# Performance work log

Measured on AMD Instinct MI355X. Metric: run time of the kernel, lower is better.

The kernel has to match this reference:

```python
import jax, jax.numpy as jnp
import numpy as np

B, T, C = 8, 512, 512
H, HKV, D = 8, 4, 64
S_MAX = 128
BASE_FREQ = 10000.0
INIT_SIGMA = 256.0
EPS = 1e-6


def _init_positional_kernel(n_heads, head_dim, s_max, base_freq):
    table_size = 2 * s_max + 1
    deltas = jnp.arange(table_size) - s_max
    d_half = head_dim // 2
    freqs = 1.0 / base_freq ** (jnp.arange(d_half, dtype=jnp.float32) / d_half)
    phases = deltas[:, None].astype(jnp.float32) * freqs[None, :]
    P_single = jnp.concatenate([jnp.cos(phases), jnp.sin(phases)], axis=-1)
    return jnp.tile(P_single[None, :, :], (n_heads, 1, 1))


def setup_inputs() -> dict:
    key = jax.random.key(0)
    ks = jax.random.split(key, 6)
    scale = 0.02
    x = jax.random.normal(ks[0], (B, T, C), dtype=jnp.float32)
    Wq = jax.random.normal(ks[1], (C, H * D), dtype=jnp.float32) * scale
    Wk = jax.random.normal(ks[2], (C, HKV * D), dtype=jnp.float32) * scale
    Wv = jax.random.normal(ks[3], (C, HKV * D), dtype=jnp.float32) * scale
    Wproj = jax.random.normal(ks[4], (C, C), dtype=jnp.float32) * scale
    P = _init_positional_kernel(H, D, S_MAX, BASE_FREQ)
    sigma = jnp.full((H,), INIT_SIGMA, dtype=jnp.float32)
    return {"x": x, "Wq": Wq, "Wk": Wk, "Wv": Wv, "Wproj": Wproj, "P": P, "sigma": sigma}


def _norm(t):
    # nGPT-style: unit norm * sqrt(dim)
    dim = t.shape[-1]
    return t * (jnp.sqrt(float(dim)) * jax.lax.rsqrt((t * t).sum(axis=-1, keepdims=True) + EPS))


def _warped_kernel(P, sigma, T_):
    # P: [H, 2*S_MAX+1, D], sigma: [H] -> P_interp: [H, T, T, D]
    positions = jnp.arange(T_)
    delta = positions[:, None] - positions[None, :]  # [T, T]
    s = jnp.abs(sigma) + 1e-6
    delta_warped = S_MAX * jnp.tanh(delta[None, :, :].astype(jnp.float32) / s[:, None, None])
    delta_table = delta_warped + S_MAX  # [H, T, T]
    idx_lo = jnp.floor(delta_table).astype(jnp.int32)
    idx_hi = idx_lo + 1
    frac = delta_table - idx_lo.astype(P.dtype)
    table_max = 2 * S_MAX
    idx_lo = jnp.clip(idx_lo, 0, table_max)
    idx_hi = jnp.clip(idx_hi, 0, table_max)
    head_idx = jnp.arange(H)[:, None, None]
    P_lo = P[head_idx, idx_lo, :]  # [H, T, T, D]
    P_hi = P[head_idx, idx_hi, :]
    return (1 - frac[..., None]) * P_lo + frac[..., None] * P_hi


def reference(x, Wq, Wk, Wv, Wproj, P, sigma):
    q = (x @ Wq).reshape(B, T, H, D)
    k = (x @ Wk).reshape(B, T, HKV, D)
    v = (x @ Wv).reshape(B, T, HKV, D)
    q, k = _norm(q), _norm(k)
    repeats = H // HKV
    k = jnp.repeat(k, repeats, axis=2)
    v = jnp.repeat(v, repeats, axis=2)
    q = q.transpose(0, 2, 1, 3)  # [B, H, T, D]
    k = k.transpose(0, 2, 1, 3)
    v = v.transpose(0, 2, 1, 3)

    sm_scale = 1.0 / jnp.sqrt(float(D))
    P_interp = _warped_kernel(P, sigma, T)  # [H, T, T, D]
    S = jnp.einsum('bhid,hijd,bhjd->bhij', q, P_interp, k) * sm_scale
    causal_mask = jnp.tril(jnp.ones((T, T), dtype=jnp.bool_))
    S = jnp.where(causal_mask[None, None, :, :], S, jnp.finfo(S.dtype).min)
    A = jax.nn.softmax(S, axis=-1)
    y = A @ v  # [B, H, T, D]
    y = y.transpose(0, 2, 1, 3).reshape(B, T, H * D)
    return y @ Wproj
```

## Files before the change

kernel.cpp:

```cpp
#include <hip/hip_runtime.h>
#include <hip/hip_bf16.h>
#include <math.h>

#define Bb 8
#define Tt 512
#define Cc 512
#define Hh 8
#define HKV 4
#define Dd 64

typedef __attribute__((ext_vector_type(8))) short short8;
typedef __attribute__((ext_vector_type(4))) float float4v;
typedef __attribute__((ext_vector_type(2))) __fp16 h2;
typedef __attribute__((ext_vector_type(8))) __fp16 half8;

__device__ __forceinline__ h2 u2h(unsigned u) {
  union { unsigned u; h2 h; } x; x.u = u; return x.h;
}
__device__ __forceinline__ unsigned h2u(h2 h) {
  union { h2 h; unsigned u; } x; x.h = h; return x.u;
}
__device__ __forceinline__ float fdot2(h2 a, h2 b, float c) {
#if __has_builtin(__builtin_amdgcn_fdot2)
  return __builtin_amdgcn_fdot2(a, b, c, false);
#else
  return fmaf((float)a.x, (float)b.x, fmaf((float)a.y, (float)b.y, c));
#endif
}

__device__ __forceinline__ float wave_reduce_sum(float v) {
#pragma unroll
  for (int off = 32; off > 0; off >>= 1) v += __shfl_xor(v, off, 64);
  return v;
}
__device__ __forceinline__ unsigned pack_bf2(float a, float b) {
  __hip_bfloat162 h = __float22bfloat162_rn(make_float2(a, b));
  return *(unsigned*)&h;
}

__global__ __launch_bounds__(256) void prep(
    const float* __restrict__ x, const float* __restrict__ Wq,
    const float* __restrict__ Wk, const float* __restrict__ Wv,
    const float* __restrict__ Wp, const float* __restrict__ P,
    const float* __restrict__ sigma,
    unsigned short* __restrict__ xb, unsigned short* __restrict__ Wtq,
    unsigned short* __restrict__ Wtp, unsigned short* __restrict__ Pwh) {
  const int bid = blockIdx.x;
  const int t = threadIdx.x;
  if (bid < 1024) {
    int i = (bid * 256 + t) * 8;
    float4 f0 = *(const float4*)&x[i];
    float4 f1 = *(const float4*)&x[i + 4];
    unsigned u[4] = {pack_bf2(f0.x, f0.y), pack_bf2(f0.z, f0.w),
                     pack_bf2(f1.x, f1.y), pack_bf2(f1.z, f1.w)};
    *(uint4*)&xb[i] = *(uint4*)u;
  } else if (bid < 1216) {
    __shared__ float Ts[64][65];
    const int bx = bid - 1024;
    const int k0 = (bx & 7) << 6;
    const int n0 = (bx >> 3) << 6;
    const float* src; int ld, nc0; unsigned short* dst; int ndst;
    if (n0 < 512)       { src = Wq; ld = 512; nc0 = n0;        dst = Wtq; ndst = n0; }
    else if (n0 < 768)  { src = Wk; ld = 256; nc0 = n0 - 512;  dst = Wtq; ndst = n0; }
    else if (n0 < 1024) { src = Wv; ld = 256; nc0 = n0 - 768;  dst = Wtq; ndst = n0; }
    else                { src = Wp; ld = 512; nc0 = n0 - 1024; dst = Wtp; ndst = n0 - 1024; }
    const int r = t >> 4, c4 = (t & 15) << 2;
#pragma unroll
    for (int rr = 0; rr < 4; ++rr) {
      int row = (rr << 4) + r;
      float4 f = *(const float4*)&src[(k0 + row) * ld + nc0 + c4];
      Ts[row][c4] = f.x; Ts[row][c4 + 1] = f.y;
      Ts[row][c4 + 2] = f.z; Ts[row][c4 + 3] = f.w;
    }
    __syncthreads();
#pragma unroll
    for (int rr = 0; rr < 4; ++rr) {
      int nr = (rr << 4) + r;
      unsigned u0 = pack_bf2(Ts[c4][nr], Ts[c4 + 1][nr]);
      unsigned u1 = pack_bf2(Ts[c4 + 2][nr], Ts[c4 + 3][nr]);
      *(uint2*)&dst[(ndst + nr) * 512 + k0 + c4] = make_uint2(u0, u1);
    }
  } else {
    int idx = (bid - 1216) * 256 + t;
    int d = idx & 63;
    int rem = idx >> 6;
    int dd = rem % 1023;
    int h = rem / 1023;
    float s = fabsf(sigma[h]) + 1e-6f;
    float delta = (float)(dd - 511);
    float dt = 128.0f * tanhf(delta / s) + 128.0f;
    float lo = floorf(dt);
    int ilo = (int)lo;
    float frac = dt - lo;
    ilo = max(0, min(ilo, 256));
    int ihi = min(ilo + 1, 256);
    const float* Pb = P + h * 257 * 64;
    float val = (1.0f - frac) * Pb[ilo * 64 + d] + frac * Pb[ihi * 64 + d];
    __fp16 hv = (__fp16)val;
    Pwh[idx] = *(unsigned short*)&hv;
  }
}

__global__ __launch_bounds__(256) void qkv_mfma(
    const unsigned short* __restrict__ xb, const unsigned short* __restrict__ Wt,
    unsigned short* __restrict__ qh, unsigned short* __restrict__ kh,
    unsigned short* __restrict__ vT) {
  __shared__ unsigned short As[64][72];
  __shared__ unsigned short Bs[64][72];
  const int m0 = blockIdx.x * 64;
  const int n0 = blockIdx.y * 64;
  const int t = threadIdx.x;
  const int w = t >> 6, lane = t & 63;
  const int srow = t >> 2, sc = (t & 3) << 4;
  float4v acc[4] = {{0,0,0,0},{0,0,0,0},{0,0,0,0},{0,0,0,0}};
  for (int k0 = 0; k0 < 512; k0 += 64) {
    uint4 a0 = *(const uint4*)&xb[(m0 + srow) * 512 + k0 + sc];
    uint4 a1 = *(const uint4*)&xb[(m0 + srow) * 512 + k0 + sc + 8];
    uint4 b0 = *(const uint4*)&Wt[(n0 + srow) * 512 + k0 + sc];
    uint4 b1 = *(const uint4*)&Wt[(n0 + srow) * 512 + k0 + sc + 8];
    __syncthreads();
    *(uint4*)&As[srow][sc] = a0; *(uint4*)&As[srow][sc + 8] = a1;
    *(uint4*)&Bs[srow][sc] = b0; *(uint4*)&Bs[srow][sc + 8] = b1;
    __syncthreads();
    const int ml = (w << 4) + (lane & 15);
    const int kq = (lane >> 4) << 3;
    short8 aF0 = *(short8*)&As[ml][kq];
    short8 aF1 = *(short8*)&As[ml][kq + 32];
#pragma unroll
    for (int nt = 0; nt < 4; ++nt) {
      const int nl = (nt << 4) + (lane & 15);
      short8 bF0 = *(short8*)&Bs[nl][kq];
      short8 bF1 = *(short8*)&Bs[nl][kq + 32];
      acc[nt] = __builtin_amdgcn_mfma_f32_16x16x32_bf16(aF0, bF0, acc[nt], 0, 0, 0);
      acc[nt] = __builtin_amdgcn_mfma_f32_16x16x32_bf16(aF1, bF1, acc[nt], 0, 0, 0);
    }
  }
  const int lane15 = lane & 15;
  const int rowbase = m0 + (w << 4) + ((lane >> 4) << 2);
  if (n0 < 768) {
#pragma unroll
    for (int r = 0; r < 4; ++r) {
      float ss = 0.0f;
#pragma unroll
      for (int nt = 0; nt < 4; ++nt) ss = fmaf(acc[nt][r], acc[nt][r], ss);
#pragma unroll
      for (int off = 1; off < 16; off <<= 1) ss += __shfl_xor(ss, off, 64);
      float sc2 = 8.0f * rsqrtf(ss + 1e-6f);
      const int row = rowbase + r;
      if (n0 < 512) {
        const int h = n0 >> 6;
        const float sc3 = sc2 * 0.125f;
#pragma unroll
        for (int nt = 0; nt < 4; ++nt) {
          __fp16 hv = (__fp16)(acc[nt][r] * sc3);
          qh[(row * Hh + h) * Dd + (nt << 4) + lane15] = *(unsigned short*)&hv;
        }
      } else {
        const int hkv = (n0 - 512) >> 6;
#pragma unroll
        for (int nt = 0; nt < 4; ++nt) {
          __fp16 hv = (__fp16)(acc[nt][r] * sc2);
          kh[(row * HKV + hkv) * Dd + (nt << 4) + lane15] = *(unsigned short*)&hv;
        }
      }
    }
  } else {
    const int hkv = (n0 - 768) >> 6;
    const int bb = rowbase >> 9;
    const int trow = rowbase & 511;
#pragma unroll
    for (int nt = 0; nt < 4; ++nt) {
      const int d = (nt << 4) + lane15;
      unsigned u0 = h2u(__builtin_amdgcn_cvt_pkrtz(acc[nt][0], acc[nt][1]));
      unsigned u1 = h2u(__builtin_amdgcn_cvt_pkrtz(acc[nt][2], acc[nt][3]));
      *(uint2*)&vT[((bb * HKV + hkv) * 64 + d) * 512 + trow] = make_uint2(u0, u1);
    }
  }
}

__global__ __launch_bounds__(256) void proj_mfma(
    const unsigned short* __restrict__ yb, const unsigned short* __restrict__ Wt,
    float* __restrict__ out) {
  __shared__ unsigned short As[64][72];
  __shared__ unsigned short Bs[64][72];
  const int m0 = blockIdx.x * 64;
  const int n0 = blockIdx.y * 64;
  const int t = threadIdx.x;
  const int w = t >> 6, lane = t & 63;
  const int srow = t >> 2, sc = (t & 3) << 4;
  float4v acc[4] = {{0,0,0,0},{0,0,0,0},{0,0,0,0},{0,0,0,0}};
  for (int k0 = 0; k0 < 512; k0 += 64) {
    uint4 a0 = *(const uint4*)&yb[(m0 + srow) * 512 + k0 + sc];
    uint4 a1 = *(const uint4*)&yb[(m0 + srow) * 512 + k0 + sc + 8];
    uint4 b0 = *(const uint4*)&Wt[(n0 + srow) * 512 + k0 + sc];
    uint4 b1 = *(const uint4*)&Wt[(n0 + srow) * 512 + k0 + sc + 8];
    __syncthreads();
    *(uint4*)&As[srow][sc] = a0; *(uint4*)&As[srow][sc + 8] = a1;
    *(uint4*)&Bs[srow][sc] = b0; *(uint4*)&Bs[srow][sc + 8] = b1;
    __syncthreads();
    const int ml = (w << 4) + (lane & 15);
    const int kq = (lane >> 4) << 3;
    short8 aF0 = *(short8*)&As[ml][kq];
    short8 aF1 = *(short8*)&As[ml][kq + 32];
#pragma unroll
    for (int nt = 0; nt < 4; ++nt) {
      const int nl = (nt << 4) + (lane & 15);
      short8 bF0 = *(short8*)&Bs[nl][kq];
      short8 bF1 = *(short8*)&Bs[nl][kq + 32];
      acc[nt] = __builtin_amdgcn_mfma_f32_16x16x32_bf16(aF0, bF0, acc[nt], 0, 0, 0);
      acc[nt] = __builtin_amdgcn_mfma_f32_16x16x32_bf16(aF1, bF1, acc[nt], 0, 0, 0);
    }
  }
#pragma unroll
  for (int nt = 0; nt < 4; ++nt) {
    int col = n0 + (nt << 4) + (lane & 15);
#pragma unroll
    for (int r = 0; r < 4; ++r) {
      int row = m0 + (w << 4) + ((lane >> 4) << 2) + r;
      out[row * 512 + col] = acc[nt][r];
    }
  }
}

__global__ __launch_bounds__(256) void attn(
    const unsigned short* __restrict__ qh, const unsigned short* __restrict__ kh,
    const unsigned short* __restrict__ vT, const unsigned short* __restrict__ Pwh,
    unsigned short* __restrict__ yb) {
  __shared__ __fp16 PwS[96][72];
  __shared__ __fp16 pS[32][72];
  __shared__ float lS[32];

  const int t = threadIdx.x;
  const int lane = t & 63;
  const int wu = __builtin_amdgcn_readfirstlane(t >> 6);
  const int bh = blockIdx.x;
  const int b = bh >> 3;
  const int h = bh & 7;
  const int hkv = h >> 1;
  const int i0 = (int)((0x4567BA983210CDEFull >> (blockIdx.y * 4)) & 15) * 32;

  float l_lane[8];
#pragma unroll
  for (int r = 0; r < 8; ++r) l_lane[r] = 0.0f;
  float4v oacc[2] = {{0, 0, 0, 0}, {0, 0, 0, 0}};

  const int prow = (wu << 3) + 63 - lane;
  const int i_base = i0 + (wu << 3);
  const unsigned short* qbase = &qh[((b * Tt + i_base) * Hh + h) * Dd];

  const int i16 = (wu & 1) << 4;
  const int dt0 = (wu >> 1) << 1;
  const int lm = lane & 15;
  const int kq = (lane >> 4) << 3;
  const unsigned short* vTbase = &vT[((b * HKV + hkv) * 64) * 512];

  for (int jt0 = 0; jt0 <= i0 + 31; jt0 += 64) {
    __syncthreads();
    {
      int jr = t >> 2, dc = (t & 3) << 4;
      const int pb0 = h * 1023 + (i0 - jt0) + 448;
      const unsigned short* pwp = &Pwh[(pb0 + jr) * 64 + dc];
      *(uint4*)&PwS[jr][dc]     = *(const uint4*)&pwp[0];
      *(uint4*)&PwS[jr][dc + 8] = *(const uint4*)&pwp[8];
      int pr2 = 64 + (t >> 3), dc2 = (t & 7) << 3;
      if (pr2 < 95)
        *(uint4*)&PwS[pr2][dc2] = *(const uint4*)&Pwh[(pb0 + pr2) * 64 + dc2];
    }
    uint4 kr[8];
    {
      const uint4* kp = (const uint4*)&kh[((b * Tt + jt0 + lane) * HKV + hkv) * Dd];
#pragma unroll
      for (int c = 0; c < 8; ++c) kr[c] = kp[c];
    }
    __syncthreads();

    const int j = jt0 + lane;
#pragma unroll
    for (int r = 0; r < 8; ++r) {
      const uint4* qp = (const uint4*)&qbase[r * (Hh * Dd)];
      float srx = 0.0f, sry = 0.0f, srz = 0.0f, srw = 0.0f;
#pragma unroll
      for (int ch = 0; ch < 8; ++ch) {
        uint4 qu = qp[ch];
        uint4 pu = *(uint4*)&PwS[prow + r][ch << 3];
        srx = fdot2(u2h(qu.x) * u2h(pu.x), u2h(kr[ch].x), srx);
        sry = fdot2(u2h(qu.y) * u2h(pu.y), u2h(kr[ch].y), sry);
        srz = fdot2(u2h(qu.z) * u2h(pu.z), u2h(kr[ch].z), srz);
        srw = fdot2(u2h(qu.w) * u2h(pu.w), u2h(kr[ch].w), srw);
      }
      float sr = (srx + sry) + (srz + srw);
      float sv = (j <= i_base + r) ? sr : -1e30f;
      float p = __expf(sv - 6.0f);
      l_lane[r] += p;
      pS[(wu << 3) + r][lane] = (__fp16)p;
    }
    __syncthreads();

    half8 a0 = *(half8*)&pS[i16 + lm][kq];
    half8 a1 = *(half8*)&pS[i16 + lm][kq + 32];
#pragma unroll
    for (int dd = 0; dd < 2; ++dd) {
      const unsigned short* vp = vTbase + (((dt0 + dd) << 4) + lm) * 512 + jt0 + kq;
      half8 b0 = *(const half8*)&vp[0];
      half8 b1 = *(const half8*)&vp[32];
      oacc[dd] = __builtin_amdgcn_mfma_f32_16x16x32_f16(a0, b0, oacc[dd], 0, 0, 0);
      oacc[dd] = __builtin_amdgcn_mfma_f32_16x16x32_f16(a1, b1, oacc[dd], 0, 0, 0);
    }
  }

#pragma unroll
  for (int r = 0; r < 8; ++r) {
    float lr = wave_reduce_sum(l_lane[r]);
    if (lane == r) lS[(wu << 3) + r] = lr;
  }
  __syncthreads();

#pragma unroll
  for (int dd = 0; dd < 2; ++dd) {
    const int d = ((dt0 + dd) << 4) + lm;
#pragma unroll
    for (int r = 0; r < 4; ++r) {
      const int irow = i16 + ((lane >> 4) << 2) + r;
      const float val = oacc[dd][r] / lS[irow];
      __hip_bfloat16 hv = __float2bfloat16(val);
      yb[((b * Tt + i0 + irow) * Hh + h) * Dd + d] = *(unsigned short*)&hv;
    }
  }
}

extern "C" void kernel_launch(void* const* d_in, const int* in_sizes, int n_in,
                              void* d_out, int out_size, void* d_ws, size_t ws_size,
                              hipStream_t stream) {
  const float* x     = (const float*)d_in[0];
  const float* Wq    = (const float*)d_in[1];
  const float* Wk    = (const float*)d_in[2];
  const float* Wv    = (const float*)d_in[3];
  const float* Wproj = (const float*)d_in[4];
  const float* P     = (const float*)d_in[5];
  const float* sigma = (const float*)d_in[6];
  float* out = (float*)d_out;

  float* ws = (float*)d_ws;
  unsigned short* qh  = (unsigned short*)ws;
  unsigned short* kh  = (unsigned short*)(ws + 1048576);
  unsigned short* vT  = (unsigned short*)(ws + 1572864);
  unsigned short* Pwh = (unsigned short*)(ws + 2097152);
  unsigned short* xb  = (unsigned short*)(ws + 2359296);
  unsigned short* yb  = xb;
  unsigned short* Wtq = (unsigned short*)(ws + 3407872);
  unsigned short* Wtp = (unsigned short*)(ws + 3670016);

  prep<<<dim3(3262), 256, 0, stream>>>(x, Wq, Wk, Wv, Wproj, P, sigma,
                                       xb, Wtq, Wtp, Pwh);
  qkv_mfma<<<dim3(64, 16), 256, 0, stream>>>(xb, Wtq, qh, kh, vT);
  attn<<<dim3(64, 16), 256, 0, stream>>>(qh, kh, vT, Pwh, yb);
  proj_mfma<<<dim3(64, 8), 256, 0, stream>>>(yb, Wtp, out);
}
```

Before: 137.6 us.

## Split long causal attention rows across two blocks and merge partial sums

Query tiles in the upper half of the sequence (yp ≥ 8) now have their key range split between two blocks. A constant table assigns each blockIdx.y a query tile, a starting key tile and a key-tile count, which caps per-block work at four key tiles instead of up to eight. Split blocks write unnormalized partial outputs and row sums to scratch space, reusing the output buffer and the no-longer-needed weight workspace. A new merge kernel adds the two halves and normalizes. The attention kernel also gets an occupancy hint of 8 blocks per SM. The aim is to remove the causal load imbalance at the tail, at the cost of an extra launch and extra global traffic for the partials.

```diff
diff --git a/kernel.cpp b/kernel.cpp
--- a/kernel.cpp
+++ b/kernel.cpp
@@ -37,6 +37,17 @@
   __hip_bfloat162 h = __float22bfloat162_rn(make_float2(a, b));
   return *(unsigned*)&h;
 }
+
+__constant__ unsigned ATAB[24] = {
+  0x04000F, 0x04000E, 0x04040F, 0x04040E, 0x04000D, 0x04000C,
+  0x03040D, 0x03040C, 0x03000B, 0x03000A, 0x03030B, 0x03030A,
+  0x030009, 0x030008,
+  0x040007, 0x040006,
+  0x020309, 0x020308,
+  0x030005, 0x030004,
+  0x020003, 0x020002,
+  0x010001, 0x010000
+};
 
 __global__ __launch_bounds__(256) void prep(
     const float* __restrict__ x, const float* __restrict__ Wq,
@@ -222,10 +233,11 @@
   }
 }
 
-__global__ __launch_bounds__(256) void attn(
+__global__ __launch_bounds__(256, 8) void attn(
     const unsigned short* __restrict__ qh, const unsigned short* __restrict__ kh,
     const unsigned short* __restrict__ vT, const unsigned short* __restrict__ Pwh,
-    unsigned short* __restrict__ yb) {
+    unsigned short* __restrict__ yb, float* __restrict__ opart,
+    float* __restrict__ lpart) {
   __shared__ __fp16 PwS[96][72];
   __shared__ __fp16 pS[32][72];
   __shared__ float lS[32];
@@ -237,7 +249,11 @@
   const int b = bh >> 3;
   const int h = bh & 7;
   const int hkv = h >> 1;
-  const int i0 = (int)((0x4567BA983210CDEFull >> (blockIdx.y * 4)) & 15) * 32;
+  const unsigned ae = ATAB[blockIdx.y];
+  const int yp  = ae & 255;
+  const int jts = (ae >> 8) & 255;
+  const int njt = (ae >> 16) & 255;
+  const int i0 = yp << 5;
 
   float l_lane[8];
 #pragma unroll
@@ -254,7 +270,8 @@
   const int kq = (lane >> 4) << 3;
   const unsigned short* vTbase = &vT[((b * HKV + hkv) * 64) * 512];
 
-  for (int jt0 = 0; jt0 <= i0 + 31; jt0 += 64) {
+  for (int jt = jts; jt < jts + njt; ++jt) {
+    const int jt0 = jt << 6;
     __syncthreads();
     {
       int jr = t >> 2, dc = (t & 3) << 4;
@@ -315,17 +332,58 @@
   }
   __syncthreads();
 
-#pragma unroll
-  for (int dd = 0; dd < 2; ++dd) {
-    const int d = ((dt0 + dd) << 4) + lm;
-#pragma unroll
-    for (int r = 0; r < 4; ++r) {
-      const int irow = i16 + ((lane >> 4) << 2) + r;
-      const float val = oacc[dd][r] / lS[irow];
-      __hip_bfloat16 hv = __float2bfloat16(val);
-      yb[((b * Tt + i0 + irow) * Hh + h) * Dd + d] = *(unsigned short*)&hv;
-    }
-  }
+  if (yp >= 8) {
+    const int slot = (jts != 0);
+    const int pbase = (((bh << 3) + (yp - 8)) << 1) + slot;
+    float* ob = opart + pbase * 2048;
+#pragma unroll
+    for (int dd = 0; dd < 2; ++dd) {
+      const int d = ((dt0 + dd) << 4) + lm;
+#pragma unroll
+      for (int r = 0; r < 4; ++r) {
+        const int irow = i16 + ((lane >> 4) << 2) + r;
+        ob[irow * 64 + d] = oacc[dd][r];
+      }
+    }
+    if (t < 32) lpart[pbase * 32 + t] = lS[t];
+  } else {
+#pragma unroll
+    for (int dd = 0; dd < 2; ++dd) {
+      const int d = ((dt0 + dd) << 4) + lm;
+#pragma unroll
+      for (int r = 0; r < 4; ++r) {
+        const int irow = i16 + ((lane >> 4) << 2) + r;
+        const float val = oacc[dd][r] / lS[irow];
+        __hip_bfloat16 hv = __float2bfloat16(val);
+        yb[((b * Tt + i0 + irow) * Hh + h) * Dd + d] = *(unsigned short*)&hv;
+      }
+    }
+  }
+}
+
+__global__ __launch_bounds__(256) void merge(
+    const float* __restrict__ opart, const float* __restrict__ lpart,
+    unsigned short* __restrict__ yb) {
+  const int bt = blockIdx.x;
+  const int bh = bt >> 3;
+  const int b = bh >> 3, h = bh & 7;
+  const int i0 = ((bt & 7) + 8) << 5;
+  const int t = threadIdx.x;
+  const int row = t >> 3;
+  const int d0 = (t & 7) << 3;
+  const float* oA = opart + (bt << 1) * 2048;
+  const float* oB = oA + 2048;
+  const float linv = 1.0f / (lpart[(bt << 1) * 32 + row] + lpart[((bt << 1) + 1) * 32 + row]);
+  float4 a0 = *(const float4*)&oA[row * 64 + d0];
+  float4 a1 = *(const float4*)&oA[row * 64 + d0 + 4];
+  float4 b0 = *(const float4*)&oB[row * 64 + d0];
+  float4 b1 = *(const float4*)&oB[row * 64 + d0 + 4];
+  unsigned u[4];
+  u[0] = pack_bf2((a0.x + b0.x) * linv, (a0.y + b0.y) * linv);
+  u[1] = pack_bf2((a0.z + b0.z) * linv, (a0.w + b0.w) * linv);
+  u[2] = pack_bf2((a1.x + b1.x) * linv, (a1.y + b1.y) * linv);
+  u[3] = pack_bf2((a1.z + b1.z) * linv, (a1.w + b1.w) * linv);
+  *(uint4*)&yb[((b * Tt + i0 + row) * Hh + h) * Dd + d0] = *(uint4*)u;
 }
 
 extern "C" void kernel_launch(void* const* d_in, const int* in_sizes, int n_in,
@@ -350,9 +408,13 @@
   unsigned short* Wtq = (unsigned short*)(ws + 3407872);
   unsigned short* Wtp = (unsigned short*)(ws + 3670016);
 
+  float* opart = out;
+  float* lpart = ws + 3407872;
+
   prep<<<dim3(3262), 256, 0, stream>>>(x, Wq, Wk, Wv, Wproj, P, sigma,
                                        xb, Wtq, Wtp, Pwh);
   qkv_mfma<<<dim3(64, 16), 256, 0, stream>>>(xb, Wtq, qh, kh, vT);
-  attn<<<dim3(64, 16), 256, 0, stream>>>(qh, kh, vT, Pwh, yb);
+  attn<<<dim3(64, 24), 256, 0, stream>>>(qh, kh, vT, Pwh, yb, opart, lpart);
+  merge<<<dim3(512), 256, 0, stream>>>(opart, lpart, yb);
   proj_mfma<<<dim3(64, 8), 256, 0, stream>>>(yb, Wtp, out);
 }
```

Result: slower. 164.6 us (+19.6%).

## Widen attention key tile to 128 and schedule query blocks largest-first

Applied to the files above, without the earlier changes.

The attention loop now processes 128 keys per iteration instead of 64. Each lane computes scores for two keys that share the same q loads, the staged positional-kernel slab grows to 159 rows, and the P·V step issues four MFMAs per d-tile instead of two. This halves the number of loop iterations and their barriers and adds more independent work per lane. The scrambled query-block ordering is replaced with a simple descending order, so the longest causal rows are scheduled first. The cost is extra masked-out work on the final partial tile, most noticeable for small i0, and higher register and LDS use, which may lower occupancy.

```diff
diff --git a/kernel.cpp b/kernel.cpp
--- a/kernel.cpp
+++ b/kernel.cpp
@@ -226,8 +226,8 @@
     const unsigned short* __restrict__ qh, const unsigned short* __restrict__ kh,
     const unsigned short* __restrict__ vT, const unsigned short* __restrict__ Pwh,
     unsigned short* __restrict__ yb) {
-  __shared__ __fp16 PwS[96][72];
-  __shared__ __fp16 pS[32][72];
+  __shared__ __fp16 PwS[160][72];
+  __shared__ __fp16 pS[32][136];
   __shared__ float lS[32];
 
   const int t = threadIdx.x;
@@ -237,14 +237,15 @@
   const int b = bh >> 3;
   const int h = bh & 7;
   const int hkv = h >> 1;
-  const int i0 = (int)((0x4567BA983210CDEFull >> (blockIdx.y * 4)) & 15) * 32;
+  const int i0 = 480 - blockIdx.y * 32;
 
   float l_lane[8];
 #pragma unroll
   for (int r = 0; r < 8; ++r) l_lane[r] = 0.0f;
   float4v oacc[2] = {{0, 0, 0, 0}, {0, 0, 0, 0}};
 
-  const int prow = (wu << 3) + 63 - lane;
+  const int prowA = (wu << 3) + 127 - lane;
+  const int prowB = (wu << 3) + 63 - lane;
   const int i_base = i0 + (wu << 3);
   const unsigned short* qbase = &qh[((b * Tt + i_base) * Hh + h) * Dd];
 
@@ -254,57 +255,75 @@
   const int kq = (lane >> 4) << 3;
   const unsigned short* vTbase = &vT[((b * HKV + hkv) * 64) * 512];
 
-  for (int jt0 = 0; jt0 <= i0 + 31; jt0 += 64) {
+  for (int jt0 = 0; jt0 < i0 + 32; jt0 += 128) {
     __syncthreads();
     {
-      int jr = t >> 2, dc = (t & 3) << 4;
-      const int pb0 = h * 1023 + (i0 - jt0) + 448;
-      const unsigned short* pwp = &Pwh[(pb0 + jr) * 64 + dc];
-      *(uint4*)&PwS[jr][dc]     = *(const uint4*)&pwp[0];
-      *(uint4*)&PwS[jr][dc + 8] = *(const uint4*)&pwp[8];
-      int pr2 = 64 + (t >> 3), dc2 = (t & 7) << 3;
-      if (pr2 < 95)
-        *(uint4*)&PwS[pr2][dc2] = *(const uint4*)&Pwh[(pb0 + pr2) * 64 + dc2];
-    }
-    uint4 kr[8];
+      const int pb0 = h * 1023 + (i0 - jt0) + 384;
+      int s = t;
+#pragma unroll
+      for (int rnd = 0; rnd < 5; ++rnd) {
+        if (s < 1272) {
+          int r = s >> 3, c = (s & 7) << 3;
+          *(uint4*)&PwS[r][c] = *(const uint4*)&Pwh[(pb0 + r) * 64 + c];
+        }
+        s += 256;
+      }
+    }
+    uint4 kra[8], krb[8];
     {
-      const uint4* kp = (const uint4*)&kh[((b * Tt + jt0 + lane) * HKV + hkv) * Dd];
-#pragma unroll
-      for (int c = 0; c < 8; ++c) kr[c] = kp[c];
-    }
-    __syncthreads();
-
-    const int j = jt0 + lane;
+      const uint4* kpa = (const uint4*)&kh[((b * Tt + jt0 + lane) * HKV + hkv) * Dd];
+      const uint4* kpb = (const uint4*)&kh[((b * Tt + jt0 + 64 + lane) * HKV + hkv) * Dd];
+#pragma unroll
+      for (int c = 0; c < 8; ++c) { kra[c] = kpa[c]; krb[c] = kpb[c]; }
+    }
+    __syncthreads();
+
+    const int ja = jt0 + lane;
+    const int jb = jt0 + 64 + lane;
 #pragma unroll
     for (int r = 0; r < 8; ++r) {
       const uint4* qp = (const uint4*)&qbase[r * (Hh * Dd)];
-      float srx = 0.0f, sry = 0.0f, srz = 0.0f, srw = 0.0f;
+      float sa = 0.0f, sb = 0.0f;
 #pragma unroll
       for (int ch = 0; ch < 8; ++ch) {
         uint4 qu = qp[ch];
-        uint4 pu = *(uint4*)&PwS[prow + r][ch << 3];
-        srx = fdot2(u2h(qu.x) * u2h(pu.x), u2h(kr[ch].x), srx);
-        sry = fdot2(u2h(qu.y) * u2h(pu.y), u2h(kr[ch].y), sry);
-        srz = fdot2(u2h(qu.z) * u2h(pu.z), u2h(kr[ch].z), srz);
-        srw = fdot2(u2h(qu.w) * u2h(pu.w), u2h(kr[ch].w), srw);
+        uint4 pa = *(uint4*)&PwS[prowA + r][ch << 3];
+        uint4 pb = *(uint4*)&PwS[prowB + r][ch << 3];
+        h2 qx = u2h(qu.x), qy = u2h(qu.y), qz = u2h(qu.z), qw = u2h(qu.w);
+        sa = fdot2(qx * u2h(pa.x), u2h(kra[ch].x), sa);
+        sa = fdot2(qy * u2h(pa.y), u2h(kra[ch].y), sa);
+        sa = fdot2(qz * u2h(pa.z), u2h(kra[ch].z), sa);
+        sa = fdot2(qw * u2h(pa.w), u2h(kra[ch].w), sa);
+        sb = fdot2(qx * u2h(pb.x), u2h(krb[ch].x), sb);
+        sb = fdot2(qy * u2h(pb.y), u2h(krb[ch].y), sb);
+        sb = fdot2(qz * u2h(pb.z), u2h(krb[ch].z), sb);
+        sb = fdot2(qw * u2h(pb.w), u2h(krb[ch].w), sb);
       }
-      float sr = (srx + sry) + (srz + srw);
-      float sv = (j <= i_base + r) ? sr : -1e30f;
-      float p = __expf(sv - 6.0f);
-      l_lane[r] += p;
-      pS[(wu << 3) + r][lane] = (__fp16)p;
+      float sva = (ja <= i_base + r) ? sa : -1e30f;
+      float svb = (jb <= i_base + r) ? sb : -1e30f;
+      float pva = __expf(sva - 6.0f);
+      float pvb = __expf(svb - 6.0f);
+      l_lane[r] += pva + pvb;
+      pS[(wu << 3) + r][lane] = (__fp16)pva;
+      pS[(wu << 3) + r][lane + 64] = (__fp16)pvb;
     }
     __syncthreads();
 
     half8 a0 = *(half8*)&pS[i16 + lm][kq];
     half8 a1 = *(half8*)&pS[i16 + lm][kq + 32];
+    half8 a2 = *(half8*)&pS[i16 + lm][kq + 64];
+    half8 a3 = *(half8*)&pS[i16 + lm][kq + 96];
 #pragma unroll
     for (int dd = 0; dd < 2; ++dd) {
       const unsigned short* vp = vTbase + (((dt0 + dd) << 4) + lm) * 512 + jt0 + kq;
       half8 b0 = *(const half8*)&vp[0];
       half8 b1 = *(const half8*)&vp[32];
+      half8 b2 = *(const half8*)&vp[64];
+      half8 b3 = *(const half8*)&vp[96];
       oacc[dd] = __builtin_amdgcn_mfma_f32_16x16x32_f16(a0, b0, oacc[dd], 0, 0, 0);
       oacc[dd] = __builtin_amdgcn_mfma_f32_16x16x32_f16(a1, b1, oacc[dd], 0, 0, 0);
+      oacc[dd] = __builtin_amdgcn_mfma_f32_16x16x32_f16(a2, b2, oacc[dd], 0, 0, 0);
+      oacc[dd] = __builtin_amdgcn_mfma_f32_16x16x32_f16(a3, b3, oacc[dd], 0, 0, 0);
     }
   }
 
```

Measured after the change: 148.2 us. 7.7% more time.
